# Performance work log

Measured on AMD Instinct MI355X. Metric: run time of the kernel, lower is better.

## Reference

```python
import jax, jax.numpy as jnp
import numpy as np

N_NODES = 100000
N_EDGES = 1600000
FEATS = 128
HIDDEN = 64
N_CLASS = 40
NEG_SLOPE = 0.01  # torch leaky_relu default


def _glorot(key, shape):
    lim = float(np.sqrt(6.0 / (shape[0] + shape[1])))
    return jax.random.uniform(key, shape, jnp.float32, -lim, lim)


def setup_inputs() -> dict:
    key = jax.random.key(0)
    ks = jax.random.split(key, 10)
    x = jax.random.normal(ks[0], (N_NODES, FEATS), jnp.float32)
    edge_index = jax.random.randint(ks[1], (2, N_EDGES), 0, N_NODES, jnp.int64)
    edge_weight = jax.random.uniform(ks[2], (N_EDGES,), jnp.float32)
    return {
        "x": x,
        "edge_index": edge_index,
        "edge_weight": edge_weight,
        "W_first": _glorot(ks[3], (FEATS, HIDDEN)),
        "b_first": jnp.zeros((HIDDEN,), jnp.float32),
        "Wc1": _glorot(ks[4], (HIDDEN, HIDDEN)),
        "bc1": jnp.zeros((HIDDEN,), jnp.float32),
        "Wc2": _glorot(ks[5], (HIDDEN, HIDDEN)),
        "bc2": jnp.zeros((HIDDEN,), jnp.float32),
        "W_out": _glorot(ks[6], (HIDDEN, N_CLASS)),
        "b_out": jnp.zeros((N_CLASS,), jnp.float32),
    }


def _gcn_norm(edge_index, edge_weight, n):
    # PyG gcn_norm with add_self_loops=True: A_hat = D^-1/2 (A + I) D^-1/2
    loop = jnp.arange(n, dtype=edge_index.dtype)
    src = jnp.concatenate([edge_index[0], loop])
    dst = jnp.concatenate([edge_index[1], loop])
    ew = jnp.concatenate([edge_weight, jnp.ones((n,), edge_weight.dtype)])
    deg = jax.ops.segment_sum(ew, dst, num_segments=n)  # degree at target
    dis = jnp.where(deg > 0, jax.lax.rsqrt(deg), 0.0)
    norm = dis[src] * ew * dis[dst]  # [E+N]
    return src, dst, norm


def _gcn_conv(h, src, dst, norm, W, b, n):
    h = h @ W                                   # [N, H]
    msg = norm[:, None] * h[src]                # gather + scale  [E+N, H]
    out = jax.ops.segment_sum(msg, dst, num_segments=n)  # scatter-add
    return out + b


def reference(x, edge_index, edge_weight, W_first, b_first, Wc1, bc1, Wc2, bc2, W_out, b_out):
    n = x.shape[0]
    src, dst, norm = _gcn_norm(edge_index, edge_weight, n)
    h = jax.nn.leaky_relu(x @ W_first + b_first, NEG_SLOPE)
    # dropout is identity in eval mode
    h = jax.nn.leaky_relu(_gcn_conv(h, src, dst, norm, Wc1, bc1, n), NEG_SLOPE)
    h = jax.nn.leaky_relu(_gcn_conv(h, src, dst, norm, Wc2, bc2, n), NEG_SLOPE)
    logits = h @ W_out + b_out
    return jax.nn.log_softmax(logits, axis=-1)
```

## Files before the change

kernel.cpp:

```cpp
#include <hip/hip_runtime.h>
#include <hip/hip_bf16.h>
#include <math.h>

#define NFEATS 128
#define NHID   64
#define NCLS   40
#define NEG_SLOPE 0.01f

#define GSH_S  9
#define GSPAN_S 512
#define GCAP_S 9216
#define SB     2048

typedef float f32x4 __attribute__((ext_vector_type(4)));
typedef int   i32x2 __attribute__((ext_vector_type(2)));

__device__ inline unsigned short f2bfu(float v) {
    union { float f; unsigned int u; } x; x.f = v;
    unsigned int r = (x.u + 0x7FFFu + ((x.u >> 16) & 1u)) >> 16;
    return (unsigned short)r;
}
__device__ inline float bf2f(unsigned short u) {
    union { unsigned int u32; float f; } x; x.u32 = ((unsigned int)u) << 16;
    return x.f;
}
__device__ inline float bflo(unsigned int u) {
    union { unsigned int v; float f; } x; x.v = u << 16; return x.f;
}
__device__ inline float bfhi(unsigned int u) {
    union { unsigned int v; float f; } x; x.v = u & 0xFFFF0000u; return x.f;
}

__device__ inline void role_split(int i, int nA, int nB, int* ia, int* ib) {
    *ia = -1; *ib = -1;
    int m2 = 2 * min(nA, nB);
    if (i < m2) { if (i & 1) *ib = i >> 1; else *ia = i >> 1; }
    else if (nA > nB) *ia = i - nB;
    else *ib = i - nA;
}


__global__ __launch_bounds__(256) void stage_gemm1_kernel(
    const int* __restrict__ srcA, const int* __restrict__ dstA, const float* __restrict__ ew,
    int* __restrict__ gcur, int2* __restrict__ staged, int E, int nStage, int ngrp,
    const float* __restrict__ x, const float* __restrict__ W1, const float* __restrict__ b1,
    float* __restrict__ h1, int n, int nTile) {
    __shared__ __align__(16) float Ws[64 * 64];

    int ia, ib;
    role_split(blockIdx.x, nStage, nTile, &ia, &ib);
    int tid = threadIdx.x;

    if (ia >= 0) {
        int* hist = (int*)Ws;
        int* wcur = ((int*)Ws) + 256;
        if (tid < 256) hist[tid] = 0;
        __syncthreads();

        int q0 = (ia * SB) >> 2;
        int qend = min(q0 + SB / 4, E >> 2);
        int dcache[8], scache[8];
        float wcache[8];

#pragma unroll
        for (int it = 0; it < 2; ++it) {
            int q = q0 + it * 256 + tid;
            bool ok = (q < qend);
            int4 d4 = ok ? ((const int4*)dstA)[q] : make_int4(-1, -1, -1, -1);
            int4 s4 = ok ? ((const int4*)srcA)[q] : make_int4(0, 0, 0, 0);
            float4 w4 = ok ? ((const float4*)ew)[q] : make_float4(0, 0, 0, 0);
            dcache[it * 4 + 0] = d4.x; dcache[it * 4 + 1] = d4.y;
            dcache[it * 4 + 2] = d4.z; dcache[it * 4 + 3] = d4.w;
            scache[it * 4 + 0] = s4.x; scache[it * 4 + 1] = s4.y;
            scache[it * 4 + 2] = s4.z; scache[it * 4 + 3] = s4.w;
            wcache[it * 4 + 0] = w4.x; wcache[it * 4 + 1] = w4.y;
            wcache[it * 4 + 2] = w4.z; wcache[it * 4 + 3] = w4.w;
#pragma unroll
            for (int j = 0; j < 4; ++j)
                if (dcache[it * 4 + j] >= 0) atomicAdd(&hist[dcache[it * 4 + j] >> GSH_S], 1);
        }
        if (ia == nStage - 1) {
            for (int e = (E & ~3) + tid; e < E; e += 256) atomicAdd(&hist[dstA[e] >> GSH_S], 1);
        }
        __syncthreads();

        if (tid < ngrp) {
            int c = hist[tid];
            wcur[tid] = (c > 0) ? atomicAdd(&gcur[tid], c) : 0;
        }
        __syncthreads();

        int pos[8];
#pragma unroll
        for (int j = 0; j < 8; ++j) {
            int d = dcache[j];
            pos[j] = (d >= 0) ? atomicAdd(&wcur[d >> GSH_S], 1) : GCAP_S;
        }
#pragma unroll
        for (int j = 0; j < 8; ++j) {
            int d = dcache[j];
            if (d >= 0 && pos[j] < GCAP_S)
                staged[(size_t)(d >> GSH_S) * GCAP_S + pos[j]] =
                    make_int2(((d & (GSPAN_S - 1)) << 17) | scache[j], __float_as_int(wcache[j]));
        }
        if (ia == nStage - 1) {
            for (int e = (E & ~3) + tid; e < E; e += 256) {
                int d = dstA[e];
                int g = d >> GSH_S;
                int p = atomicAdd(&wcur[g], 1);
                if (p < GCAP_S)
                    staged[(size_t)g * GCAP_S + p] =
                        make_int2(((d & (GSPAN_S - 1)) << 17) | srcA[e], __float_as_int(ew[e]));
            }
        }
        return;
    }

    int c4 = (tid & 15) * 4;
    int r0 = ib * 64 + (tid >> 4) * 4;
    int rr[4];
#pragma unroll
    for (int i = 0; i < 4; ++i) rr[i] = min(r0 + i, n - 1);

    float acc[4][4] = {};
    for (int ph = 0; ph < 2; ++ph) {
        __syncthreads();
        for (int i = tid; i < 64 * 16; i += 256)
            ((float4*)Ws)[i] = ((const float4*)W1)[ph * 1024 + i];
        __syncthreads();
#pragma unroll 2
        for (int kk = 0; kk < 64; kk += 4) {
            f32x4 av[4], bv[4];
#pragma unroll
            for (int i = 0; i < 4; ++i)
                av[i] = __builtin_nontemporal_load(
                    (const f32x4*)&x[(size_t)rr[i] * NFEATS + ph * 64 + kk]);
#pragma unroll
            for (int q = 0; q < 4; ++q) bv[q] = *(const f32x4*)&Ws[(kk + q) * 64 + c4];
#pragma unroll
            for (int i = 0; i < 4; ++i) {
#pragma unroll
                for (int q = 0; q < 4; ++q) {
                    float a = av[i][q];
#pragma unroll
                    for (int j = 0; j < 4; ++j) acc[i][j] += a * bv[q][j];
                }
            }
        }
    }

#pragma unroll
    for (int i = 0; i < 4; ++i) {
        int rw = r0 + i;
        if (rw >= n) break;
        float4 o;
        float* oa = (float*)&o;
#pragma unroll
        for (int j = 0; j < 4; ++j) {
            float v = acc[i][j] + b1[c4 + j];
            oa[j] = (v > 0.0f) ? v : v * NEG_SLOPE;
        }
        *(float4*)&h1[(size_t)rw * 64 + c4] = o;
    }
}


__global__ __launch_bounds__(512) void deg_dis_kernel(const int* __restrict__ gcur,
                                                      const int2* __restrict__ staged,
                                                      float* __restrict__ dis, int n) {
    __shared__ float deg[GSPAN_S];
    int tid = threadIdx.x;
    int g = blockIdx.x;
    deg[tid] = 0.0f;
    __syncthreads();

    int cnt = min(gcur[g], GCAP_S);
    const i32x2* sl = (const i32x2*)(staged + (size_t)g * GCAP_S);
    for (int i = tid; i < cnt; i += 512) {
        i32x2 r = sl[i];
        atomicAdd(&deg[r[0] >> 17], __int_as_float(r[1]));
    }
    __syncthreads();

    int node = g * GSPAN_S + tid;
    if (node < n) dis[node] = rsqrtf(1.0f + deg[tid]);
}


__global__ __launch_bounds__(512) void sort_gemm2_kernel(
    const int* __restrict__ gcur, const int2* __restrict__ staged,
    int2* __restrict__ staged2, const float* __restrict__ dis,
    int2* __restrict__ nodeptr, int ngrp,
    const float* __restrict__ in, const float* __restrict__ W,
    unsigned short* __restrict__ outp, int n, int nTile2) {
    __shared__ __align__(16) float Ws[NHID * 64];
    __shared__ int hist[GSPAN_S], base[GSPAN_S], cur[GSPAN_S];
    __shared__ float disl[GSPAN_S];

    int ia, ib;
    role_split(blockIdx.x, ngrp, nTile2, &ia, &ib);
    int tid = threadIdx.x;

    if (ia >= 0) {
        int g = ia;
        int cnt = min(gcur[g], GCAP_S);
        const int2* sl = staged + (size_t)g * GCAP_S;
        hist[tid] = 0;
        int node = g * GSPAN_S + tid;
        disl[tid] = (node < n) ? dis[node] : 0.0f;
        __syncthreads();
        for (int i = tid; i < cnt; i += 512) atomicAdd(&hist[sl[i].x >> 17], 1);
        __syncthreads();
        base[tid] = hist[tid];
        __syncthreads();
        for (int off = 1; off < GSPAN_S; off <<= 1) {
            int t_ = (tid >= off) ? base[tid - off] : 0;
            __syncthreads();
            base[tid] += t_;
            __syncthreads();
        }
        int ex = base[tid] - hist[tid];
        cur[tid] = ex;
        if (node < n) nodeptr[node] = make_int2(g * GCAP_S + ex, hist[tid]);
        __syncthreads();
        int2* out = staged2 + (size_t)g * GCAP_S;
        for (int i = tid; i < cnt; i += 512) {
            int2 r = sl[i];
            int dl = r.x >> 17, s = r.x & 0x1FFFF;
            float w = dis[s] * __int_as_float(r.y) * disl[dl];
            int pos = atomicAdd(&cur[dl], 1);
            out[pos] = make_int2(s, __float_as_int(w));
        }
        return;
    }

    for (int i = tid; i < NHID * 16; i += 512) ((float4*)Ws)[i] = ((const float4*)W)[i];
    __syncthreads();

    int half = tid >> 8;
    int t2 = tid & 255;
    int tile = ib * 2 + half;
    int c4 = (t2 & 15) * 4;
    int r0 = tile * 64 + (t2 >> 4) * 4;
    int rr[4];
#pragma unroll
    for (int i = 0; i < 4; ++i) rr[i] = min(r0 + i, n - 1);

    float acc[4][4] = {};
#pragma unroll 2
    for (int kk = 0; kk < NHID; kk += 4) {
        f32x4 av[4], bv[4];
#pragma unroll
        for (int i = 0; i < 4; ++i)
            av[i] = __builtin_nontemporal_load((const f32x4*)&in[(size_t)rr[i] * NHID + kk]);
#pragma unroll
        for (int q = 0; q < 4; ++q) bv[q] = *(const f32x4*)&Ws[(kk + q) * 64 + c4];
#pragma unroll
        for (int i = 0; i < 4; ++i) {
#pragma unroll
            for (int q = 0; q < 4; ++q) {
                float a = av[i][q];
#pragma unroll
                for (int j = 0; j < 4; ++j) acc[i][j] += a * bv[q][j];
            }
        }
    }

#pragma unroll
    for (int i = 0; i < 4; ++i) {
        int rw = r0 + i;
        if (rw >= n) break;
        ushort4 o;
        o.x = f2bfu(acc[i][0]); o.y = f2bfu(acc[i][1]);
        o.z = f2bfu(acc[i][2]); o.w = f2bfu(acc[i][3]);
        *(ushort4*)&outp[(size_t)rw * 64 + c4] = o;
    }
}


template <int LAYER>
__global__ __launch_bounds__(256) void agg_kernel(const int2* __restrict__ nodeptr,
                                                  const int2* __restrict__ recs0,
                                                  const unsigned short* __restrict__ tb,
                                                  const float* __restrict__ dis,
                                                  const float* __restrict__ bias,
                                                  unsigned short* __restrict__ outp, int n) {
    int wv = threadIdx.x >> 6;
    int lane = threadIdx.x & 63;
    int node = blockIdx.x * 4 + wv;
    if (node >= n) return;

    int2 np = nodeptr[node];
    int start = np.x, c = np.y;
    int grp = lane >> 4;
    int r16 = lane & 15;
    float di = dis[node];

    f32x4 a0 = {0, 0, 0, 0}, a1 = {0, 0, 0, 0}, a2 = {0, 0, 0, 0}, a3 = {0, 0, 0, 0};

    if (grp == 0) {
        uint2 uv = *(const uint2*)&tb[(size_t)node * NHID + r16 * 4];
        float d2 = di * di;
        a0[0] += d2 * bflo(uv.x); a0[1] += d2 * bfhi(uv.x);
        a0[2] += d2 * bflo(uv.y); a0[3] += d2 * bfhi(uv.y);
    }

    const i32x2* recs = (const i32x2*)(recs0 + start);
    for (int b = 0; b < c; b += 64) {
        int rem = min(64, c - b);
        i32x2 ent = (lane < rem) ? recs[b + lane] : (i32x2){0, 0};
        for (int k = 0; k < rem; k += 16) {
            int e0 = k + grp, e1 = k + 4 + grp, e2 = k + 8 + grp, e3 = k + 12 + grp;
            int s0 = __shfl(ent[0], e0); float w0 = __int_as_float(__shfl(ent[1], e0));
            int s1 = __shfl(ent[0], e1); float w1 = __int_as_float(__shfl(ent[1], e1));
            int s2 = __shfl(ent[0], e2); float w2 = __int_as_float(__shfl(ent[1], e2));
            int s3 = __shfl(ent[0], e3); float w3 = __int_as_float(__shfl(ent[1], e3));
            uint2 u0 = *(const uint2*)&tb[(size_t)s0 * NHID + r16 * 4];
            uint2 u1 = *(const uint2*)&tb[(size_t)s1 * NHID + r16 * 4];
            uint2 u2 = *(const uint2*)&tb[(size_t)s2 * NHID + r16 * 4];
            uint2 u3 = *(const uint2*)&tb[(size_t)s3 * NHID + r16 * 4];
            a0[0] += w0 * bflo(u0.x); a0[1] += w0 * bfhi(u0.x);
            a0[2] += w0 * bflo(u0.y); a0[3] += w0 * bfhi(u0.y);
            a1[0] += w1 * bflo(u1.x); a1[1] += w1 * bfhi(u1.x);
            a1[2] += w1 * bflo(u1.y); a1[3] += w1 * bfhi(u1.y);
            a2[0] += w2 * bflo(u2.x); a2[1] += w2 * bfhi(u2.x);
            a2[2] += w2 * bflo(u2.y); a2[3] += w2 * bfhi(u2.y);
            a3[0] += w3 * bflo(u3.x); a3[1] += w3 * bfhi(u3.x);
            a3[2] += w3 * bflo(u3.y); a3[3] += w3 * bfhi(u3.y);
        }
    }

    f32x4 acc;
#pragma unroll
    for (int j = 0; j < 4; ++j) acc[j] = (a0[j] + a1[j]) + (a2[j] + a3[j]);
#pragma unroll
    for (int j = 0; j < 4; ++j) {
        acc[j] += __shfl_xor(acc[j], 16);
        acc[j] += __shfl_xor(acc[j], 32);
    }

    if (lane < 16) {
        ushort4 o;
        unsigned short* op = (unsigned short*)&o;
#pragma unroll
        for (int j = 0; j < 4; ++j) {
            float v = acc[j];
            if (LAYER == 1) {
                v += bias[r16 * 4 + j];
                v = (v > 0.0f) ? v : v * NEG_SLOPE;
            }
            op[j] = f2bfu(v);
        }
        *(ushort4*)&outp[(size_t)node * NHID + r16 * 4] = o;
    }
}


__global__ __launch_bounds__(256) void tail_kernel(const unsigned short* __restrict__ ub,
                                                   const float* __restrict__ Wc2,
                                                   const float* __restrict__ bc2,
                                                   const float* __restrict__ Wo,
                                                   const float* __restrict__ bo,
                                                   float* __restrict__ outp, int n) {
    __shared__ __align__(16) float WsA[NHID * 64];
    __shared__ __align__(16) unsigned short hs[64 * 68];
    __shared__ float bos[NCLS];

    int tid = threadIdx.x;
    for (int i = tid; i < NHID * 16; i += 256) ((float4*)WsA)[i] = ((const float4*)Wc2)[i];
    __syncthreads();

    int c4 = (tid & 15) * 4;
    int r0l = (tid >> 4) * 4;
    int base = blockIdx.x * 64;

    int rr[4];
#pragma unroll
    for (int i = 0; i < 4; ++i) rr[i] = min(base + r0l + i, n - 1);

    float acc[4][4] = {};
#pragma unroll 2
    for (int kk = 0; kk < NHID; kk += 4) {
        f32x4 av[4], bv[4];
#pragma unroll
        for (int i = 0; i < 4; ++i) {
            ushort4 uv = *(const ushort4*)&ub[(size_t)rr[i] * NHID + kk];
            av[i][0] = bf2f(uv.x); av[i][1] = bf2f(uv.y);
            av[i][2] = bf2f(uv.z); av[i][3] = bf2f(uv.w);
        }
#pragma unroll
        for (int q = 0; q < 4; ++q) bv[q] = *(const f32x4*)&WsA[(kk + q) * 64 + c4];
#pragma unroll
        for (int i = 0; i < 4; ++i) {
#pragma unroll
            for (int q = 0; q < 4; ++q) {
                float a = av[i][q];
#pragma unroll
                for (int j = 0; j < 4; ++j) acc[i][j] += a * bv[q][j];
            }
        }
    }

#pragma unroll
    for (int i = 0; i < 4; ++i) {
#pragma unroll
        for (int j = 0; j < 4; ++j) {
            float v = acc[i][j] + bc2[c4 + j];
            v = (v > 0.0f) ? v : v * NEG_SLOPE;
            hs[(r0l + i) * 68 + c4 + j] = f2bfu(v);
        }
    }
    __syncthreads();

    for (int i = tid; i < NHID * NCLS / 4; i += 256) ((float4*)WsA)[i] = ((const float4*)Wo)[i];
    if (tid < NCLS) bos[tid] = bo[tid];
    __syncthreads();

    int row = tid >> 2;
    int c0 = (tid & 3) * 10;
    int node = base + row;

    float z[10];
#pragma unroll
    for (int j = 0; j < 10; ++j) z[j] = 0.0f;

#pragma unroll 2
    for (int k0 = 0; k0 < NHID; k0 += 4) {
        ushort4 hv = *(const ushort4*)&hs[row * 68 + k0];
        float h0 = bf2f(hv.x), h1 = bf2f(hv.y), h2 = bf2f(hv.z), h3 = bf2f(hv.w);
        const float* w0 = &WsA[(k0 + 0) * NCLS + c0];
        const float* w1 = &WsA[(k0 + 1) * NCLS + c0];
        const float* w2 = &WsA[(k0 + 2) * NCLS + c0];
        const float* w3 = &WsA[(k0 + 3) * NCLS + c0];
#pragma unroll
        for (int j = 0; j < 10; ++j)
            z[j] += h0 * w0[j] + h1 * w1[j] + h2 * w2[j] + h3 * w3[j];
    }
#pragma unroll
    for (int j = 0; j < 10; ++j) z[j] += bos[c0 + j];

    float m = z[0];
#pragma unroll
    for (int j = 1; j < 10; ++j) m = fmaxf(m, z[j]);
    m = fmaxf(m, __shfl_xor(m, 1));
    m = fmaxf(m, __shfl_xor(m, 2));

    float s = 0.0f;
#pragma unroll
    for (int j = 0; j < 10; ++j) s += expf(z[j] - m);
    s += __shfl_xor(s, 1);
    s += __shfl_xor(s, 2);
    float ls = logf(s);

    if (node < n) {
#pragma unroll
        for (int j = 0; j < 10; ++j)
            outp[(size_t)node * NCLS + c0 + j] = z[j] - m - ls;
    }
}


extern "C" void kernel_launch(void* const* d_in, const int* in_sizes, int n_in,
                              void* d_out, int out_size, void* d_ws, size_t ws_size,
                              hipStream_t stream) {
    const float* x   = (const float*)d_in[0];
    const int*   ei  = (const int*)d_in[1];
    const float* ew  = (const float*)d_in[2];
    const float* W1  = (const float*)d_in[3];
    const float* b1  = (const float*)d_in[4];
    const float* Wc1 = (const float*)d_in[5];
    const float* bc1 = (const float*)d_in[6];
    const float* Wc2 = (const float*)d_in[7];
    const float* bc2 = (const float*)d_in[8];
    const float* Wo  = (const float*)d_in[9];
    const float* bo  = (const float*)d_in[10];
    float* out = (float*)d_out;

    const int N = in_sizes[0] / NFEATS;
    const int E = in_sizes[1] / 2;
    const int* src = ei;
    const int* dst = ei + E;

    const int ngrp   = (N + GSPAN_S - 1) >> GSH_S;
    const int nStage = (E + SB - 1) / SB;
    const int nTile  = (N + 63) / 64;
    const int nTile2 = (N + 127) / 128;
    const int aggBlocks = (N + 3) / 4;

    float*          bufA  = (float*)d_ws;
    unsigned short* t1b   = (unsigned short*)(bufA + (size_t)N * NHID);
    unsigned short* h2b   = t1b + (size_t)N * NHID;
    int2*  staged  = (int2*)(h2b + (size_t)N * NHID);
    int2*  staged2 = staged + (size_t)ngrp * GCAP_S;
    float* dis     = (float*)(staged2 + (size_t)ngrp * GCAP_S);
    int*   gcur    = (int*)(dis + N);
    int2*  nodeptr = (int2*)(gcur + ((ngrp + 1) & ~1));

    hipMemsetAsync(gcur, 0, ngrp * sizeof(int), stream);

    stage_gemm1_kernel<<<nStage + nTile, 256, 0, stream>>>(
        src, dst, ew, gcur, staged, E, nStage, ngrp, x, W1, b1, bufA, N, nTile);

    deg_dis_kernel<<<ngrp, 512, 0, stream>>>(gcur, staged, dis, N);

    sort_gemm2_kernel<<<ngrp + nTile2, 512, 0, stream>>>(
        gcur, staged, staged2, dis, nodeptr, ngrp, bufA, Wc1, t1b, N, nTile2);

    agg_kernel<1><<<aggBlocks, 256, 0, stream>>>(nodeptr, staged2, t1b, dis, bc1, h2b, N);

    agg_kernel<2><<<aggBlocks, 256, 0, stream>>>(nodeptr, staged2, h2b, dis, nullptr, t1b, N);

    tail_kernel<<<nTile, 256, 0, stream>>>(t1b, Wc2, bc2, Wo, bo, out, N);
}
```

Baseline: 271.1 us.

## Fold degree normalization into node features and merge degree with sort

The per-edge weight dis[src]*w*dis[dst] is factored out. The GEMM2 output rows are pre-scaled by dis[src], and the aggregation result is scaled by dis[dst], with layer 1 also scaling its output for the next layer. This lets the degree computation and the bucket sort run in one kernel, since the sort no longer needs dis, and it removes the random dis gathers per edge. The cost is a separate GEMM2 launch instead of a role-split fused launch, plus extra bf16 rounding of pre-scaled features.

```diff
diff --git a/kernel.cpp b/kernel.cpp
--- a/kernel.cpp
+++ b/kernel.cpp
@@ -165,83 +165,67 @@
 }
 
 
-__global__ __launch_bounds__(512) void deg_dis_kernel(const int* __restrict__ gcur,
-                                                      const int2* __restrict__ staged,
-                                                      float* __restrict__ dis, int n) {
+__global__ __launch_bounds__(512) void degsort_kernel(
+    const int* __restrict__ gcur, const int2* __restrict__ staged,
+    int2* __restrict__ staged2, float* __restrict__ dis,
+    int2* __restrict__ nodeptr, int n) {
     __shared__ float deg[GSPAN_S];
+    __shared__ int hist[GSPAN_S], base[GSPAN_S], cur[GSPAN_S];
+
     int tid = threadIdx.x;
     int g = blockIdx.x;
     deg[tid] = 0.0f;
+    hist[tid] = 0;
     __syncthreads();
 
     int cnt = min(gcur[g], GCAP_S);
-    const i32x2* sl = (const i32x2*)(staged + (size_t)g * GCAP_S);
+    const int2* sl = staged + (size_t)g * GCAP_S;
     for (int i = tid; i < cnt; i += 512) {
-        i32x2 r = sl[i];
-        atomicAdd(&deg[r[0] >> 17], __int_as_float(r[1]));
+        int2 r = sl[i];
+        int dl = r.x >> 17;
+        atomicAdd(&deg[dl], __int_as_float(r.y));
+        atomicAdd(&hist[dl], 1);
     }
     __syncthreads();
 
     int node = g * GSPAN_S + tid;
     if (node < n) dis[node] = rsqrtf(1.0f + deg[tid]);
-}
-
-
-__global__ __launch_bounds__(512) void sort_gemm2_kernel(
-    const int* __restrict__ gcur, const int2* __restrict__ staged,
-    int2* __restrict__ staged2, const float* __restrict__ dis,
-    int2* __restrict__ nodeptr, int ngrp,
-    const float* __restrict__ in, const float* __restrict__ W,
-    unsigned short* __restrict__ outp, int n, int nTile2) {
+
+    base[tid] = hist[tid];
+    __syncthreads();
+    for (int off = 1; off < GSPAN_S; off <<= 1) {
+        int t_ = (tid >= off) ? base[tid - off] : 0;
+        __syncthreads();
+        base[tid] += t_;
+        __syncthreads();
+    }
+    int ex = base[tid] - hist[tid];
+    base[tid] = ex;
+    cur[tid] = ex;
+    __syncthreads();
+
+    if (node < n) nodeptr[node] = make_int2(g * GCAP_S + ex, hist[tid]);
+
+    int2* out = staged2 + (size_t)g * GCAP_S;
+    for (int i = tid; i < cnt; i += 512) {
+        int2 r = sl[i];
+        int dl = r.x >> 17;
+        int pos = atomicAdd(&cur[dl], 1);
+        out[pos] = make_int2(r.x & 0x1FFFF, r.y);
+    }
+}
+
+
+__global__ __launch_bounds__(256) void gemm2s_kernel(
+    const float* __restrict__ in, const float* __restrict__ W, const float* __restrict__ dis,
+    unsigned short* __restrict__ outp, int n) {
     __shared__ __align__(16) float Ws[NHID * 64];
-    __shared__ int hist[GSPAN_S], base[GSPAN_S], cur[GSPAN_S];
-    __shared__ float disl[GSPAN_S];
-
-    int ia, ib;
-    role_split(blockIdx.x, ngrp, nTile2, &ia, &ib);
     int tid = threadIdx.x;
-
-    if (ia >= 0) {
-        int g = ia;
-        int cnt = min(gcur[g], GCAP_S);
-        const int2* sl = staged + (size_t)g * GCAP_S;
-        hist[tid] = 0;
-        int node = g * GSPAN_S + tid;
-        disl[tid] = (node < n) ? dis[node] : 0.0f;
-        __syncthreads();
-        for (int i = tid; i < cnt; i += 512) atomicAdd(&hist[sl[i].x >> 17], 1);
-        __syncthreads();
-        base[tid] = hist[tid];
-        __syncthreads();
-        for (int off = 1; off < GSPAN_S; off <<= 1) {
-            int t_ = (tid >= off) ? base[tid - off] : 0;
-            __syncthreads();
-            base[tid] += t_;
-            __syncthreads();
-        }
-        int ex = base[tid] - hist[tid];
-        cur[tid] = ex;
-        if (node < n) nodeptr[node] = make_int2(g * GCAP_S + ex, hist[tid]);
-        __syncthreads();
-        int2* out = staged2 + (size_t)g * GCAP_S;
-        for (int i = tid; i < cnt; i += 512) {
-            int2 r = sl[i];
-            int dl = r.x >> 17, s = r.x & 0x1FFFF;
-            float w = dis[s] * __int_as_float(r.y) * disl[dl];
-            int pos = atomicAdd(&cur[dl], 1);
-            out[pos] = make_int2(s, __float_as_int(w));
-        }
-        return;
-    }
-
-    for (int i = tid; i < NHID * 16; i += 512) ((float4*)Ws)[i] = ((const float4*)W)[i];
-    __syncthreads();
-
-    int half = tid >> 8;
-    int t2 = tid & 255;
-    int tile = ib * 2 + half;
-    int c4 = (t2 & 15) * 4;
-    int r0 = tile * 64 + (t2 >> 4) * 4;
+    for (int i = tid; i < NHID * 16; i += 256) ((float4*)Ws)[i] = ((const float4*)W)[i];
+    __syncthreads();
+
+    int c4 = (tid & 15) * 4;
+    int r0 = blockIdx.x * 64 + (tid >> 4) * 4;
     int rr[4];
 #pragma unroll
     for (int i = 0; i < 4; ++i) rr[i] = min(r0 + i, n - 1);
@@ -270,9 +254,10 @@
     for (int i = 0; i < 4; ++i) {
         int rw = r0 + i;
         if (rw >= n) break;
+        float dr = dis[rw];
         ushort4 o;
-        o.x = f2bfu(acc[i][0]); o.y = f2bfu(acc[i][1]);
-        o.z = f2bfu(acc[i][2]); o.w = f2bfu(acc[i][3]);
+        o.x = f2bfu(dr * acc[i][0]); o.y = f2bfu(dr * acc[i][1]);
+        o.z = f2bfu(dr * acc[i][2]); o.w = f2bfu(dr * acc[i][3]);
         *(ushort4*)&outp[(size_t)rw * 64 + c4] = o;
     }
 }
@@ -300,9 +285,8 @@
 
     if (grp == 0) {
         uint2 uv = *(const uint2*)&tb[(size_t)node * NHID + r16 * 4];
-        float d2 = di * di;
-        a0[0] += d2 * bflo(uv.x); a0[1] += d2 * bfhi(uv.x);
-        a0[2] += d2 * bflo(uv.y); a0[3] += d2 * bfhi(uv.y);
+        a0[0] += bflo(uv.x); a0[1] += bfhi(uv.x);
+        a0[2] += bflo(uv.y); a0[3] += bfhi(uv.y);
     }
 
     const i32x2* recs = (const i32x2*)(recs0 + start);
@@ -344,10 +328,13 @@
         unsigned short* op = (unsigned short*)&o;
 #pragma unroll
         for (int j = 0; j < 4; ++j) {
-            float v = acc[j];
+            float v;
             if (LAYER == 1) {
-                v += bias[r16 * 4 + j];
+                v = di * acc[j] + bias[r16 * 4 + j];
                 v = (v > 0.0f) ? v : v * NEG_SLOPE;
+                v *= di;
+            } else {
+                v = di * acc[j];
             }
             op[j] = f2bfu(v);
         }
@@ -484,7 +471,6 @@
     const int ngrp   = (N + GSPAN_S - 1) >> GSH_S;
     const int nStage = (E + SB - 1) / SB;
     const int nTile  = (N + 63) / 64;
-    const int nTile2 = (N + 127) / 128;
     const int aggBlocks = (N + 3) / 4;
 
     float*          bufA  = (float*)d_ws;
@@ -501,10 +487,9 @@
     stage_gemm1_kernel<<<nStage + nTile, 256, 0, stream>>>(
         src, dst, ew, gcur, staged, E, nStage, ngrp, x, W1, b1, bufA, N, nTile);
 
-    deg_dis_kernel<<<ngrp, 512, 0, stream>>>(gcur, staged, dis, N);
-
-    sort_gemm2_kernel<<<ngrp + nTile2, 512, 0, stream>>>(
-        gcur, staged, staged2, dis, nodeptr, ngrp, bufA, Wc1, t1b, N, nTile2);
+    degsort_kernel<<<ngrp, 512, 0, stream>>>(gcur, staged, staged2, dis, nodeptr, N);
+
+    gemm2s_kernel<<<nTile, 256, 0, stream>>>(bufA, Wc1, dis, t1b, N);
 
     agg_kernel<1><<<aggBlocks, 256, 0, stream>>>(nodeptr, staged2, t1b, dis, bc1, h2b, N);
 
```

After: 240.8 us. 1.13x faster.
